# Kernel tuning notes

Hardware: AMD Instinct MI355X
Metric: run time of the kernel (lower is better)

The kernel has to match this reference:

```python
import jax, jax.numpy as jnp
import numpy as np

B, S, E, H = 2, 2048, 1024, 16
D = E // H  # head_dim = 64
EPS = 1e-6


def _angle_decay():
    # angle: 1/10000**linspace(0,1,D//2), each value repeated twice (interleaved)
    a = 1.0 / (10000.0 ** jnp.linspace(0.0, 1.0, D // 2))
    angle = jnp.repeat(a, 2)  # [D]
    decay = jnp.log(1.0 - 2.0 ** (-5.0 - jnp.arange(H, dtype=jnp.float32)))  # [H]
    return angle, decay


def _rel_pos(slen):
    angle, decay = _angle_decay()
    idx = jnp.arange(slen, dtype=jnp.float32)
    sin = jnp.sin(idx[:, None] * angle[None, :])  # [S, D]
    cos = jnp.cos(idx[:, None] * angle[None, :])  # [S, D]
    diff = idx[:, None] - idx[None, :]            # [S, S]
    tril = diff >= 0
    masked = jnp.where(tril, diff, jnp.inf)
    mask = jnp.exp(masked * decay[:, None, None])  # [H, S, S]; exp(-inf)=0 on upper tri
    mask = jnp.nan_to_num(mask)
    mask = mask / jnp.sqrt(jnp.sum(mask, axis=-1, keepdims=True))
    return sin, cos, mask


def _rotate_every_two(x):
    x1 = x[..., ::2]
    x2 = x[..., 1::2]
    return jnp.stack((-x2, x1), axis=-1).reshape(x.shape)


def _theta_shift(x, sin, cos):
    # x: [B, H, S, D]; sin/cos: [S, D] broadcast over B,H
    return x * cos + _rotate_every_two(x) * sin


def setup_inputs() -> dict:
    key = jax.random.key(0)
    ks = jax.random.split(key, 5)
    scale = 1.0 / np.sqrt(E)
    return {
        "x": jax.random.normal(ks[0], (B, S, E), dtype=jnp.float32),
        "Wq": jax.random.normal(ks[1], (E, E), dtype=jnp.float32) * scale,
        "Wk": jax.random.normal(ks[2], (E, E), dtype=jnp.float32) * scale,
        "Wv": jax.random.normal(ks[3], (E, E), dtype=jnp.float32) * scale,
        "Wg": jax.random.normal(ks[4], (E, E), dtype=jnp.float32) * scale,
    }


def reference(x, Wq, Wk, Wv, Wg):
    bsz, tgt_len, _ = x.shape
    sin, cos, mask = _rel_pos(tgt_len)
    scaling = E ** (-0.5)

    q = x @ Wq
    k = (x @ Wk) * scaling
    v = x @ Wv
    g = x @ Wg

    q = q.reshape(bsz, tgt_len, H, D).transpose(0, 2, 1, 3)  # [B,H,S,D]
    k = k.reshape(bsz, tgt_len, H, D).transpose(0, 2, 1, 3)
    vr = v.reshape(bsz, tgt_len, H, D).transpose(0, 2, 1, 3)

    qr = _theta_shift(q, sin, cos)
    kr = _theta_shift(k, sin, cos)

    qk = jnp.einsum("bhqd,bhkd->bhqk", qr, kr) * mask[None]
    denom = jax.lax.stop_gradient(
        jnp.clip(jnp.sum(jnp.abs(qk), axis=-1, keepdims=True), 1.0, 5e4)
    )
    out = jnp.einsum("bhqk,bhkd->bhqd", qk / denom, vr)
    out = out.transpose(0, 2, 1, 3)  # [B,S,H,D]

    # RMSNorm over head_dim (no affine)
    out = out * jax.lax.rsqrt(jnp.mean(out * out, axis=-1, keepdims=True) + EPS)
    out = out.reshape(bsz, tgt_len, E)
    return jax.nn.silu(g) * out
```

## Files before the change

kernel.cpp:

```cpp
#include <hip/hip_runtime.h>

typedef unsigned short u16;
typedef __attribute__((ext_vector_type(8))) __bf16 bf16x8;
typedef __attribute__((ext_vector_type(4))) float f32x4;

#define B_SZ   2
#define S_LEN  2048
#define E_DIM  1024
#define NHEAD  16
#define HD     64
#define KDIM   1024
#define NOUT   4096

__device__ __forceinline__ float bf2f(u16 u){
  union { unsigned int i; float f; } c; c.i = ((unsigned int)u) << 16; return c.f;
}
__device__ __forceinline__ u16 f2bf(float f){
  union { float f; unsigned int i; } c; c.f = f;
  return (u16)((c.i + 0x7FFFu + ((c.i >> 16) & 1u)) >> 16);
}
__device__ __forceinline__ u16 f2bf_fast(float f){
  union { float f; unsigned int i; } c; c.f = f;
  return (u16)((c.i + 0x8000u) >> 16);
}
__device__ __forceinline__ void gl2lds16(const void* g, void* l){
  __builtin_amdgcn_global_load_lds((const __attribute__((address_space(1))) void*)g,
                                   (__attribute__((address_space(3))) void*)l, 16, 0, 0);
}

__global__ __launch_bounds__(256) void castx_kernel(const float* __restrict__ x, u16* __restrict__ xb){
  size_t flat = ((size_t)blockIdx.x * 256 + threadIdx.x) * 16;
  int m7 = (int)((flat >> 10) & 7);
  int cb = (int)((flat >> 3) & 7);
  size_t tile = flat & ~(size_t)63;
  float f[16];
  #pragma unroll
  for (int c = 0; c < 4; c++) *(float4*)&f[c * 4] = *(const float4*)&x[flat + c * 4];
  u16 o[16];
  #pragma unroll
  for (int i = 0; i < 16; i++) o[i] = f2bf(f[i]);
  *(uint4*)&xb[tile + ((cb ^ m7) * 8)]       = *(uint4*)&o[0];
  *(uint4*)&xb[tile + (((cb + 1) ^ m7) * 8)] = *(uint4*)&o[8];
}

__global__ __launch_bounds__(256) void wtrans_kernel(const float* __restrict__ Wq, const float* __restrict__ Wk,
                                                     const float* __restrict__ Wv, const float* __restrict__ Wg,
                                                     u16* __restrict__ WT){
  const float* Ws[4] = {Wq, Wk, Wv, Wg};
  const float* W = Ws[blockIdx.z];
  int n0 = blockIdx.x * 64, k0 = blockIdx.y * 64;
  __shared__ u16 tile[64][66];
  int t = threadIdx.x;
  int r = t >> 2, cg = (t & 3) * 16;
  const float* src = W + (size_t)(k0 + r) * E_DIM + n0 + cg;
  float f[16];
  #pragma unroll
  for (int c = 0; c < 4; c++) *(float4*)&f[c * 4] = *(const float4*)&src[c * 4];
  #pragma unroll
  for (int i = 0; i < 16; i++) tile[r][cg + i] = f2bf(f[i]);
  __syncthreads();
  u16 ov[16];
  #pragma unroll
  for (int i = 0; i < 16; i++) ov[i] = tile[cg + i][r];
  int n7 = r & 7, cb = cg >> 3;
  u16* dst = WT + (size_t)(blockIdx.z * E_DIM + n0 + r) * KDIM + k0;
  *(uint4*)&dst[(cb ^ n7) * 8]       = *(uint4*)&ov[0];
  *(uint4*)&dst[((cb + 1) ^ n7) * 8] = *(uint4*)&ov[8];
}

__global__ __launch_bounds__(256) void gemm_kernel(const u16* __restrict__ A, const u16* __restrict__ Bt,
                                                   u16* __restrict__ C){
  __shared__ __align__(16) u16 As[128 * 64];
  __shared__ __align__(16) u16 Bs[128 * 64];
  int m0 = blockIdx.y * 128, n0 = blockIdx.x * 128;
  int t = threadIdx.x;
  int wave = t >> 6, lane = t & 63;
  int l15 = lane & 15, quad = lane >> 4, h8 = lane & 7;
  int r0 = (wave & 1) * 64, c0 = (wave >> 1) * 64;
  f32x4 acc[4][4];
  #pragma unroll
  for (int i = 0; i < 4; i++)
    #pragma unroll
    for (int j = 0; j < 4; j++) acc[i][j] = (f32x4){0.f, 0.f, 0.f, 0.f};

  for (int k0 = 0; k0 < KDIM; k0 += 64){
    __syncthreads();
    #pragma unroll
    for (int c = 0; c < 4; c++){
      int L = c * 256 + t;
      gl2lds16(A + (size_t)(m0 + (L >> 3)) * KDIM + k0 + (L & 7) * 8, &As[L * 8]);
    }
    #pragma unroll
    for (int c = 0; c < 4; c++){
      int L = c * 256 + t;
      gl2lds16(Bt + (size_t)(n0 + (L >> 3)) * KDIM + k0 + (L & 7) * 8, &Bs[L * 8]);
    }
    __syncthreads();
    #pragma unroll
    for (int kk = 0; kk < 2; kk++){
      bf16x8 a[4], b[4];
      #pragma unroll
      for (int i = 0; i < 4; i++) a[i] = *(const bf16x8*)&As[(r0 + i * 16 + l15) * 64 + ((kk * 4 + quad) ^ h8) * 8];
      #pragma unroll
      for (int j = 0; j < 4; j++) b[j] = *(const bf16x8*)&Bs[(c0 + j * 16 + l15) * 64 + ((kk * 4 + quad) ^ h8) * 8];
      #pragma unroll
      for (int i = 0; i < 4; i++)
        #pragma unroll
        for (int j = 0; j < 4; j++)
          acc[i][j] = __builtin_amdgcn_mfma_f32_16x16x32_bf16(a[i], b[j], acc[i][j], 0, 0, 0);
    }
  }
  #pragma unroll
  for (int i = 0; i < 4; i++){
    int row = m0 + r0 + i * 16 + quad * 4;
    #pragma unroll
    for (int j = 0; j < 4; j++){
      int col = n0 + c0 + j * 16 + l15;
      #pragma unroll
      for (int r = 0; r < 4; r++)
        C[(size_t)(row + r) * NOUT + col] = f2bf(acc[i][j][r]);
    }
  }
}

__global__ __launch_bounds__(256) void shift_kernel(const u16* __restrict__ qkvg,
                                                    u16* __restrict__ qr, u16* __restrict__ kr,
                                                    u16* __restrict__ vt){
  int sb = blockIdx.x, bh = blockIdx.y;
  int s0 = sb * 64;
  int t = threadIdx.x;
  int sl = t >> 2, dg = (t & 3) * 16;
  int s = s0 + sl;
  int h = bh & 15;
  size_t token = (size_t)(bh >> 4) * S_LEN + s;
  size_t base = token * NOUT + h * HD + dg;
  u16 qv[16], kv[16], vv[16];
  *(uint4*)&qv[0] = *(const uint4*)&qkvg[base];
  *(uint4*)&qv[8] = *(const uint4*)&qkvg[base + 8];
  *(uint4*)&kv[0] = *(const uint4*)&qkvg[base + 1024];
  *(uint4*)&kv[8] = *(const uint4*)&qkvg[base + 1024 + 8];
  *(uint4*)&vv[0] = *(const uint4*)&qkvg[base + 2048];
  *(uint4*)&vv[8] = *(const uint4*)&qkvg[base + 2048 + 8];
  u16 qo[16], ko[16];
  #pragma unroll
  for (int i = 0; i < 8; i++){
    int dd = dg + 2 * i;
    float a = exp2f(-(float)(dd >> 1) * (13.287712379549449f / 31.0f));
    float ang = (float)s * a;
    float sn = sinf(ang), cs = cosf(ang);
    float qe = bf2f(qv[2 * i]), qd = bf2f(qv[2 * i + 1]);
    qo[2 * i]     = f2bf(qe * cs - qd * sn);
    qo[2 * i + 1] = f2bf(qd * cs + qe * sn);
    float ke = bf2f(kv[2 * i]) * 0.03125f, kd = bf2f(kv[2 * i + 1]) * 0.03125f;
    ko[2 * i]     = f2bf(ke * cs - kd * sn);
    ko[2 * i + 1] = f2bf(kd * cs + ke * sn);
  }
  size_t dsto = ((size_t)bh * S_LEN + s) * HD;
  *(uint4*)&qr[dsto + dg]     = *(uint4*)&qo[0];
  *(uint4*)&qr[dsto + dg + 8] = *(uint4*)&qo[8];
  int s7 = s & 7, cbk = dg >> 3;
  *(uint4*)&kr[dsto + ((cbk ^ s7) * 8)]       = *(uint4*)&ko[0];
  *(uint4*)&kr[dsto + (((cbk + 1) ^ s7) * 8)] = *(uint4*)&ko[8];
  __shared__ u16 vs[64][66];
  #pragma unroll
  for (int i = 0; i < 16; i++) vs[sl][dg + i] = vv[i];
  __syncthreads();
  int d = t >> 2, jg = (t & 3) * 16;
  u16 ov[16];
  #pragma unroll
  for (int i = 0; i < 16; i++) ov[i] = vs[jg + i][d];
  int d7 = d & 7, cbv = jg >> 3;
  size_t vrow = ((size_t)bh * HD + d) * S_LEN + s0;
  *(uint4*)&vt[vrow + ((cbv ^ d7) * 8)]       = *(uint4*)&ov[0];
  *(uint4*)&vt[vrow + (((cbv + 1) ^ d7) * 8)] = *(uint4*)&ov[8];
}

__global__ __launch_bounds__(256, 2) void retention_kernel(const u16* __restrict__ qr, const u16* __restrict__ kr,
                                                           const u16* __restrict__ vt, const u16* __restrict__ qkvg,
                                                           float* __restrict__ out){
  int bh = blockIdx.x;
  int qb = 15 - (int)blockIdx.y;
  int b = bh >> 4, h = bh & 15;
  int q0 = qb * 128;
  __shared__ __align__(16) u16 Ks[64 * 64];
  __shared__ __align__(16) u16 Vs[64 * 64];
  __shared__ __align__(16) u16 Ps[128 * 72];
  int t = threadIdx.x, wave = t >> 6, lane = t & 63;
  int l15 = lane & 15, quad = lane >> 4, h8 = lane & 7;

  float decay = log1pf(-exp2f(-5.0f - (float)h));
  float negd = -decay;
  float estep = __expf(64.0f * negd);

  int qsE[2]; int rowbase[2];
  #pragma unroll
  for (int e = 0; e < 2; e++){ rowbase[e] = wave * 32 + e * 16; qsE[e] = q0 + rowbase[e]; }

  bf16x8 aqa[2], aqb[2];
  #pragma unroll
  for (int e = 0; e < 2; e++){
    size_t qrow = ((size_t)bh * S_LEN + qsE[e] + l15) * HD;
    aqa[e] = *(const bf16x8*)&qr[qrow + quad * 8];
    aqb[e] = *(const bf16x8*)&qr[qrow + 32 + quad * 8];
  }

  float cf[4];
  #pragma unroll
  for (int ct = 0; ct < 4; ct++) cf[ct] = __expf((float)(ct * 16 + l15) * negd);

  float em1d = expm1f(decay);
  float win_f = 18.0f / negd;
  int win_i = (win_f > 2.1e9f) ? 0x7f000000 : (int)win_f;
  int jmin = q0 - win_i;
  int kb_start = jmin > 0 ? (jmin >> 6) : 0;
  int k0s = kb_start * 64;
  int qi[2][4]; float rf[2][4];
  #pragma unroll
  for (int e = 0; e < 2; e++)
    #pragma unroll
    for (int r = 0; r < 4; r++){
      qi[e][r] = qsE[e] + quad * 4 + r;
      float rowsum = expm1f((float)(qi[e][r] + 1) * decay) / em1d;
      float rinv = rsqrtf(rowsum);
      rf[e][r] = __expf((float)(qi[e][r] - k0s) * decay) * rinv;
    }

  f32x4 o[2][4];
  #pragma unroll
  for (int e = 0; e < 2; e++)
    #pragma unroll
    for (int dt = 0; dt < 4; dt++) o[e][dt] = (f32x4){0.f, 0.f, 0.f, 0.f};
  float babs[2][4] = {{0.f,0.f,0.f,0.f},{0.f,0.f,0.f,0.f}};

  const u16* krbh = kr + (size_t)bh * S_LEN * HD;
  const u16* vtbh = vt + (size_t)bh * HD * S_LEN;
  int kbend = 2 * qb + 1;

  for (int kb = kb_start; kb <= kbend; kb++){
    int k0 = kb * 64;
    __syncthreads();
    #pragma unroll
    for (int c = 0; c < 2; c++){
      int L = c * 256 + t;
      gl2lds16(krbh + (size_t)(k0) * HD + L * 8, &Ks[L * 8]);
    }
    #pragma unroll
    for (int c = 0; c < 2; c++){
      int L = c * 256 + t;
      gl2lds16(vtbh + (size_t)(L >> 3) * S_LEN + k0 + (L & 7) * 8, &Vs[L * 8]);
    }
    __syncthreads();

    bf16x8 bk0[4], bk1[4];
    #pragma unroll
    for (int ct = 0; ct < 4; ct++){
      int rw = (ct * 16 + l15) * 64;
      bk0[ct] = *(const bf16x8*)&Ks[rw + ((quad ^ h8) * 8)];
      bk1[ct] = *(const bf16x8*)&Ks[rw + (((quad + 4) ^ h8) * 8)];
    }
    #pragma unroll
    for (int e = 0; e < 2; e++){
      int qs = qsE[e];
      if (k0 <= qs + 15 && k0 + 63 >= qs - win_i){
        bool diag = (k0 + 64 > qs);
        #pragma unroll
        for (int ct = 0; ct < 4; ct++){
          f32x4 z = (f32x4){0.f, 0.f, 0.f, 0.f};
          z = __builtin_amdgcn_mfma_f32_16x16x32_bf16(aqa[e], bk0[ct], z, 0, 0, 0);
          z = __builtin_amdgcn_mfma_f32_16x16x32_bf16(aqb[e], bk1[ct], z, 0, 0, 0);
          int j = k0 + ct * 16 + l15;
          #pragma unroll
          for (int r = 0; r < 4; r++){
            float p = z[r] * (rf[e][r] * cf[ct]);
            if (diag && j > qi[e][r]) p = 0.f;
            babs[e][r] += fabsf(p);
            Ps[(rowbase[e] + quad * 4 + r) * 72 + ct * 16 + l15] = f2bf_fast(p);
          }
        }
      }
    }
    #pragma unroll
    for (int e = 0; e < 2; e++){
      int qs = qsE[e];
      if (k0 <= qs + 15 && k0 + 63 >= qs - win_i){
        bf16x8 ap0 = *(const bf16x8*)&Ps[(rowbase[e] + l15) * 72 + quad * 8];
        bf16x8 ap1 = *(const bf16x8*)&Ps[(rowbase[e] + l15) * 72 + 32 + quad * 8];
        #pragma unroll
        for (int dt = 0; dt < 4; dt++){
          int rw = (dt * 16 + l15) * 64;
          bf16x8 bv0 = *(const bf16x8*)&Vs[rw + ((quad ^ h8) * 8)];
          bf16x8 bv1 = *(const bf16x8*)&Vs[rw + (((quad + 4) ^ h8) * 8)];
          o[e][dt] = __builtin_amdgcn_mfma_f32_16x16x32_bf16(ap0, bv0, o[e][dt], 0, 0, 0);
          o[e][dt] = __builtin_amdgcn_mfma_f32_16x16x32_bf16(ap1, bv1, o[e][dt], 0, 0, 0);
        }
      }
    }
    #pragma unroll
    for (int e = 0; e < 2; e++)
      #pragma unroll
      for (int r = 0; r < 4; r++) rf[e][r] *= estep;
  }

  #pragma unroll
  for (int e = 0; e < 2; e++){
    float dinv[4];
    #pragma unroll
    for (int r = 0; r < 4; r++){
      float v = babs[e][r];
      v += __shfl_xor(v, 1); v += __shfl_xor(v, 2);
      v += __shfl_xor(v, 4); v += __shfl_xor(v, 8);
      dinv[r] = 1.0f / fminf(fmaxf(v, 1.0f), 50000.0f);
    }
    float ssq[4] = {0.f, 0.f, 0.f, 0.f};
    #pragma unroll
    for (int dt = 0; dt < 4; dt++)
      #pragma unroll
      for (int r = 0; r < 4; r++){
        float v = o[e][dt][r] * dinv[r];
        o[e][dt][r] = v;
        ssq[r] += v * v;
      }
    #pragma unroll
    for (int r = 0; r < 4; r++){
      float v = ssq[r];
      v += __shfl_xor(v, 1); v += __shfl_xor(v, 2);
      v += __shfl_xor(v, 4); v += __shfl_xor(v, 8);
      ssq[r] = rsqrtf(v * (1.0f / 64.0f) + 1e-6f);
    }
    #pragma unroll
    for (int r = 0; r < 4; r++){
      int s = qi[e][r];
      size_t gbase = ((size_t)b * S_LEN + s) * NOUT + 3072 + h * HD;
      size_t obase = ((size_t)b * S_LEN + s) * E_DIM + h * HD;
      #pragma unroll
      for (int dt = 0; dt < 4; dt++){
        int d = dt * 16 + l15;
        float gv = bf2f(qkvg[gbase + d]);
        float sg = gv / (1.0f + __expf(-gv));
        out[obase + d] = o[e][dt][r] * ssq[r] * sg;
      }
    }
  }
}

extern "C" void kernel_launch(void* const* d_in, const int* in_sizes, int n_in,
                              void* d_out, int out_size, void* d_ws, size_t ws_size,
                              hipStream_t stream){
  const float* x  = (const float*)d_in[0];
  const float* Wq = (const float*)d_in[1];
  const float* Wk = (const float*)d_in[2];
  const float* Wv = (const float*)d_in[3];
  const float* Wg = (const float*)d_in[4];
  float* out = (float*)d_out;
  char* ws = (char*)d_ws;
  u16* xb   = (u16*)(ws);
  u16* WT   = (u16*)(ws + (8ull  << 20));
  u16* qkvg = (u16*)(ws + (16ull << 20));
  u16* qrp  = (u16*)(ws);
  u16* vtp  = (u16*)(ws + (8ull  << 20));
  u16* krp  = (u16*)(ws + (48ull << 20));

  castx_kernel    <<<dim3(1024),      256, 0, stream>>>(x, xb);
  wtrans_kernel   <<<dim3(16, 16, 4), 256, 0, stream>>>(Wq, Wk, Wv, Wg, WT);
  gemm_kernel     <<<dim3(32, 32),    256, 0, stream>>>(xb, WT, qkvg);
  shift_kernel    <<<dim3(32, 32),    256, 0, stream>>>(qkvg, qrp, krp, vtp);
  retention_kernel<<<dim3(32, 16),    256, 0, stream>>>(qrp, krp, vtp, qkvg, out);
}
```

Before: 199.4 us.

## Split retention key range across two blocks and combine partials in separate kernel

Splits each retention query block's key loop into two halves (z dimension) so twice as many blocks run, writing partial outputs and abs-sums to workspace. A new combine kernel sums the partials, applies the denominator clamp, RMSNorm and SiLU gate. The gate is copied into a compact buffer during the shift pass, and the QK MFMA operands are swapped so each lane owns one query row, giving packed P stores. This adds workspace traffic and an extra launch in exchange for better load balance and occupancy.

```diff
diff --git a/kernel.cpp b/kernel.cpp
--- a/kernel.cpp
+++ b/kernel.cpp
@@ -1,6 +1,7 @@
 #include <hip/hip_runtime.h>
 
 typedef unsigned short u16;
+typedef unsigned int u32;
 typedef __attribute__((ext_vector_type(8))) __bf16 bf16x8;
 typedef __attribute__((ext_vector_type(4))) float f32x4;
 
@@ -13,14 +14,14 @@
 #define NOUT   4096
 
 __device__ __forceinline__ float bf2f(u16 u){
-  union { unsigned int i; float f; } c; c.i = ((unsigned int)u) << 16; return c.f;
+  union { u32 i; float f; } c; c.i = ((u32)u) << 16; return c.f;
 }
 __device__ __forceinline__ u16 f2bf(float f){
-  union { float f; unsigned int i; } c; c.f = f;
+  union { float f; u32 i; } c; c.f = f;
   return (u16)((c.i + 0x7FFFu + ((c.i >> 16) & 1u)) >> 16);
 }
 __device__ __forceinline__ u16 f2bf_fast(float f){
-  union { float f; unsigned int i; } c; c.f = f;
+  union { float f; u32 i; } c; c.f = f;
   return (u16)((c.i + 0x8000u) >> 16);
 }
 __device__ __forceinline__ void gl2lds16(const void* g, void* l){
@@ -125,7 +126,7 @@
 
 __global__ __launch_bounds__(256) void shift_kernel(const u16* __restrict__ qkvg,
                                                     u16* __restrict__ qr, u16* __restrict__ kr,
-                                                    u16* __restrict__ vt){
+                                                    u16* __restrict__ vt, u16* __restrict__ gc){
   int sb = blockIdx.x, bh = blockIdx.y;
   int s0 = sb * 64;
   int t = threadIdx.x;
@@ -134,13 +135,18 @@
   int h = bh & 15;
   size_t token = (size_t)(bh >> 4) * S_LEN + s;
   size_t base = token * NOUT + h * HD + dg;
-  u16 qv[16], kv[16], vv[16];
+  u16 qv[16], kv[16], vv[16], gv[16];
   *(uint4*)&qv[0] = *(const uint4*)&qkvg[base];
   *(uint4*)&qv[8] = *(const uint4*)&qkvg[base + 8];
   *(uint4*)&kv[0] = *(const uint4*)&qkvg[base + 1024];
   *(uint4*)&kv[8] = *(const uint4*)&qkvg[base + 1024 + 8];
   *(uint4*)&vv[0] = *(const uint4*)&qkvg[base + 2048];
   *(uint4*)&vv[8] = *(const uint4*)&qkvg[base + 2048 + 8];
+  *(uint4*)&gv[0] = *(const uint4*)&qkvg[base + 3072];
+  *(uint4*)&gv[8] = *(const uint4*)&qkvg[base + 3072 + 8];
+  size_t gdst = token * E_DIM + h * HD + dg;
+  *(uint4*)&gc[gdst]     = *(uint4*)&gv[0];
+  *(uint4*)&gc[gdst + 8] = *(uint4*)&gv[8];
   u16 qo[16], ko[16];
   #pragma unroll
   for (int i = 0; i < 8; i++){
@@ -176,11 +182,12 @@
 }
 
 __global__ __launch_bounds__(256, 2) void retention_kernel(const u16* __restrict__ qr, const u16* __restrict__ kr,
-                                                           const u16* __restrict__ vt, const u16* __restrict__ qkvg,
-                                                           float* __restrict__ out){
+                                                           const u16* __restrict__ vt,
+                                                           float* __restrict__ pO, float* __restrict__ pBa){
   int bh = blockIdx.x;
   int qb = 15 - (int)blockIdx.y;
-  int b = bh >> 4, h = bh & 15;
+  int z  = blockIdx.z;
+  int h = bh & 15;
   int q0 = qb * 128;
   __shared__ __align__(16) u16 Ks[64 * 64];
   __shared__ __align__(16) u16 Vs[64 * 64];
@@ -192,57 +199,61 @@
   float negd = -decay;
   float estep = __expf(64.0f * negd);
 
-  int qsE[2]; int rowbase[2];
-  #pragma unroll
-  for (int e = 0; e < 2; e++){ rowbase[e] = wave * 32 + e * 16; qsE[e] = q0 + rowbase[e]; }
-
-  bf16x8 aqa[2], aqb[2];
+  int qsE[2], rowb[2];
+  #pragma unroll
+  for (int e = 0; e < 2; e++){ rowb[e] = wave * 32 + e * 16; qsE[e] = q0 + rowb[e]; }
+
+  bf16x8 qB[2][2];
   #pragma unroll
   for (int e = 0; e < 2; e++){
     size_t qrow = ((size_t)bh * S_LEN + qsE[e] + l15) * HD;
-    aqa[e] = *(const bf16x8*)&qr[qrow + quad * 8];
-    aqb[e] = *(const bf16x8*)&qr[qrow + 32 + quad * 8];
-  }
-
-  float cf[4];
-  #pragma unroll
-  for (int ct = 0; ct < 4; ct++) cf[ct] = __expf((float)(ct * 16 + l15) * negd);
-
-  float em1d = expm1f(decay);
+    qB[e][0] = *(const bf16x8*)&qr[qrow + quad * 8];
+    qB[e][1] = *(const bf16x8*)&qr[qrow + 32 + quad * 8];
+  }
+
   float win_f = 18.0f / negd;
   int win_i = (win_f > 2.1e9f) ? 0x7f000000 : (int)win_f;
-  int jmin = q0 - win_i;
-  int kb_start = jmin > 0 ? (jmin >> 6) : 0;
-  int k0s = kb_start * 64;
-  int qi[2][4]; float rf[2][4];
+  int z_lo = z ? (qb + 1) : 0;
+  int z_hi = z ? (2 * qb + 1) : qb;
+  int kb_lo = z_lo;
+  {
+    int jmin = q0 - win_i;
+    if (jmin > z_lo * 64){ int wlo = jmin >> 6; kb_lo = wlo > z_lo ? wlo : z_lo; }
+  }
+  int k0s = kb_lo * 64;
+
+  float em1d = expm1f(decay);
+  float rfE[2]; int iE[2];
+  #pragma unroll
+  for (int e = 0; e < 2; e++){
+    int i = qsE[e] + l15;
+    iE[e] = i;
+    float rowsum = expm1f((float)(i + 1) * decay) / em1d;
+    rfE[e] = __expf((float)(i - k0s) * decay) * rsqrtf(rowsum);
+  }
+  float e1 = __expf(negd);
+  float c16 = __expf(negd * 16.0f);
+  float cbr[4];
+  cbr[0] = __expf(negd * (float)(quad * 4));
+  cbr[1] = cbr[0] * e1; cbr[2] = cbr[1] * e1; cbr[3] = cbr[2] * e1;
+
+  f32x4 o[2][4];
   #pragma unroll
   for (int e = 0; e < 2; e++)
     #pragma unroll
-    for (int r = 0; r < 4; r++){
-      qi[e][r] = qsE[e] + quad * 4 + r;
-      float rowsum = expm1f((float)(qi[e][r] + 1) * decay) / em1d;
-      float rinv = rsqrtf(rowsum);
-      rf[e][r] = __expf((float)(qi[e][r] - k0s) * decay) * rinv;
-    }
-
-  f32x4 o[2][4];
-  #pragma unroll
-  for (int e = 0; e < 2; e++)
-    #pragma unroll
     for (int dt = 0; dt < 4; dt++) o[e][dt] = (f32x4){0.f, 0.f, 0.f, 0.f};
-  float babs[2][4] = {{0.f,0.f,0.f,0.f},{0.f,0.f,0.f,0.f}};
+  float babs[2] = {0.f, 0.f};
 
   const u16* krbh = kr + (size_t)bh * S_LEN * HD;
   const u16* vtbh = vt + (size_t)bh * HD * S_LEN;
-  int kbend = 2 * qb + 1;
-
-  for (int kb = kb_start; kb <= kbend; kb++){
+
+  for (int kb = kb_lo; kb <= z_hi; kb++){
     int k0 = kb * 64;
     __syncthreads();
     #pragma unroll
     for (int c = 0; c < 2; c++){
       int L = c * 256 + t;
-      gl2lds16(krbh + (size_t)(k0) * HD + L * 8, &Ks[L * 8]);
+      gl2lds16(krbh + (size_t)k0 * HD + L * 8, &Ks[L * 8]);
     }
     #pragma unroll
     for (int c = 0; c < 2; c++){
@@ -251,31 +262,36 @@
     }
     __syncthreads();
 
-    bf16x8 bk0[4], bk1[4];
+    bf16x8 kA0[4], kA1[4];
     #pragma unroll
     for (int ct = 0; ct < 4; ct++){
       int rw = (ct * 16 + l15) * 64;
-      bk0[ct] = *(const bf16x8*)&Ks[rw + ((quad ^ h8) * 8)];
-      bk1[ct] = *(const bf16x8*)&Ks[rw + (((quad + 4) ^ h8) * 8)];
+      kA0[ct] = *(const bf16x8*)&Ks[rw + ((quad ^ h8) * 8)];
+      kA1[ct] = *(const bf16x8*)&Ks[rw + (((quad + 4) ^ h8) * 8)];
     }
     #pragma unroll
     for (int e = 0; e < 2; e++){
       int qs = qsE[e];
       if (k0 <= qs + 15 && k0 + 63 >= qs - win_i){
         bool diag = (k0 + 64 > qs);
+        float cf[4] = {cbr[0], cbr[1], cbr[2], cbr[3]};
         #pragma unroll
         for (int ct = 0; ct < 4; ct++){
-          f32x4 z = (f32x4){0.f, 0.f, 0.f, 0.f};
-          z = __builtin_amdgcn_mfma_f32_16x16x32_bf16(aqa[e], bk0[ct], z, 0, 0, 0);
-          z = __builtin_amdgcn_mfma_f32_16x16x32_bf16(aqb[e], bk1[ct], z, 0, 0, 0);
-          int j = k0 + ct * 16 + l15;
+          f32x4 zacc = (f32x4){0.f, 0.f, 0.f, 0.f};
+          zacc = __builtin_amdgcn_mfma_f32_16x16x32_bf16(kA0[ct], qB[e][0], zacc, 0, 0, 0);
+          zacc = __builtin_amdgcn_mfma_f32_16x16x32_bf16(kA1[ct], qB[e][1], zacc, 0, 0, 0);
+          u16 pk[4];
           #pragma unroll
           for (int r = 0; r < 4; r++){
-            float p = z[r] * (rf[e][r] * cf[ct]);
-            if (diag && j > qi[e][r]) p = 0.f;
-            babs[e][r] += fabsf(p);
-            Ps[(rowbase[e] + quad * 4 + r) * 72 + ct * 16 + l15] = f2bf_fast(p);
+            float p = zacc[r] * (rfE[e] * cf[r]);
+            if (diag && (k0 + ct * 16 + quad * 4 + r) > iE[e]) p = 0.f;
+            babs[e] += fabsf(p);
+            pk[r] = f2bf_fast(p);
+            cf[r] *= c16;
           }
+          u32 lo = (u32)pk[0] | ((u32)pk[1] << 16);
+          u32 hi = (u32)pk[2] | ((u32)pk[3] << 16);
+          *(uint2*)&Ps[(rowb[e] + l15) * 72 + ct * 16 + quad * 4] = make_uint2(lo, hi);
         }
       }
     }
@@ -283,64 +299,76 @@
     for (int e = 0; e < 2; e++){
       int qs = qsE[e];
       if (k0 <= qs + 15 && k0 + 63 >= qs - win_i){
-        bf16x8 ap0 = *(const bf16x8*)&Ps[(rowbase[e] + l15) * 72 + quad * 8];
-        bf16x8 ap1 = *(const bf16x8*)&Ps[(rowbase[e] + l15) * 72 + 32 + quad * 8];
+        bf16x8 pB0 = *(const bf16x8*)&Ps[(rowb[e] + l15) * 72 + quad * 8];
+        bf16x8 pB1 = *(const bf16x8*)&Ps[(rowb[e] + l15) * 72 + 32 + quad * 8];
         #pragma unroll
         for (int dt = 0; dt < 4; dt++){
           int rw = (dt * 16 + l15) * 64;
-          bf16x8 bv0 = *(const bf16x8*)&Vs[rw + ((quad ^ h8) * 8)];
-          bf16x8 bv1 = *(const bf16x8*)&Vs[rw + (((quad + 4) ^ h8) * 8)];
-          o[e][dt] = __builtin_amdgcn_mfma_f32_16x16x32_bf16(ap0, bv0, o[e][dt], 0, 0, 0);
-          o[e][dt] = __builtin_amdgcn_mfma_f32_16x16x32_bf16(ap1, bv1, o[e][dt], 0, 0, 0);
+          bf16x8 vA0 = *(const bf16x8*)&Vs[rw + ((quad ^ h8) * 8)];
+          bf16x8 vA1 = *(const bf16x8*)&Vs[rw + (((quad + 4) ^ h8) * 8)];
+          o[e][dt] = __builtin_amdgcn_mfma_f32_16x16x32_bf16(vA0, pB0, o[e][dt], 0, 0, 0);
+          o[e][dt] = __builtin_amdgcn_mfma_f32_16x16x32_bf16(vA1, pB1, o[e][dt], 0, 0, 0);
         }
       }
     }
     #pragma unroll
-    for (int e = 0; e < 2; e++)
-      #pragma unroll
-      for (int r = 0; r < 4; r++) rf[e][r] *= estep;
-  }
-
+    for (int e = 0; e < 2; e++) rfE[e] *= estep;
+  }
+
+  size_t slot = ((size_t)bh * 16 + qb) * 2 + z;
+  float* po = pO + slot * (4 * 128 * 16);
   #pragma unroll
   for (int e = 0; e < 2; e++){
-    float dinv[4];
-    #pragma unroll
-    for (int r = 0; r < 4; r++){
-      float v = babs[e][r];
-      v += __shfl_xor(v, 1); v += __shfl_xor(v, 2);
-      v += __shfl_xor(v, 4); v += __shfl_xor(v, 8);
-      dinv[r] = 1.0f / fminf(fmaxf(v, 1.0f), 50000.0f);
-    }
-    float ssq[4] = {0.f, 0.f, 0.f, 0.f};
+    float bsum = babs[e];
+    bsum += __shfl_xor(bsum, 16);
+    bsum += __shfl_xor(bsum, 32);
+    if (quad == 0) pBa[slot * 128 + rowb[e] + l15] = bsum;
     #pragma unroll
     for (int dt = 0; dt < 4; dt++)
-      #pragma unroll
-      for (int r = 0; r < 4; r++){
-        float v = o[e][dt][r] * dinv[r];
-        o[e][dt][r] = v;
-        ssq[r] += v * v;
-      }
-    #pragma unroll
-    for (int r = 0; r < 4; r++){
-      float v = ssq[r];
-      v += __shfl_xor(v, 1); v += __shfl_xor(v, 2);
-      v += __shfl_xor(v, 4); v += __shfl_xor(v, 8);
-      ssq[r] = rsqrtf(v * (1.0f / 64.0f) + 1e-6f);
-    }
-    #pragma unroll
-    for (int r = 0; r < 4; r++){
-      int s = qi[e][r];
-      size_t gbase = ((size_t)b * S_LEN + s) * NOUT + 3072 + h * HD;
-      size_t obase = ((size_t)b * S_LEN + s) * E_DIM + h * HD;
-      #pragma unroll
-      for (int dt = 0; dt < 4; dt++){
-        int d = dt * 16 + l15;
-        float gv = bf2f(qkvg[gbase + d]);
-        float sg = gv / (1.0f + __expf(-gv));
-        out[obase + d] = o[e][dt][r] * ssq[r] * sg;
-      }
-    }
-  }
+      *(float4*)&po[(dt * 128 + rowb[e] + l15) * 16 + quad * 4] = *(float4*)&o[e][dt];
+  }
+}
+
+__global__ __launch_bounds__(128) void combine_kernel(const float* __restrict__ pO, const float* __restrict__ pBa,
+                                                      const u16* __restrict__ gc, float* __restrict__ out){
+  int bh = blockIdx.x, qb = blockIdx.y;
+  int b = bh >> 4, h = bh & 15;
+  int i = threadIdx.x;
+  int s = qb * 128 + i;
+  size_t s2 = ((size_t)bh * 16 + qb) * 2;
+  const float* p0 = pO + s2 * 8192;
+  const float* p1 = p0 + 8192;
+  float v[64];
+  #pragma unroll
+  for (int dt = 0; dt < 4; dt++)
+    #pragma unroll
+    for (int c = 0; c < 4; c++){
+      float4 a  = *(const float4*)&p0[(dt * 128 + i) * 16 + c * 4];
+      float4 bb = *(const float4*)&p1[(dt * 128 + i) * 16 + c * 4];
+      int d = dt * 16 + c * 4;
+      v[d + 0] = a.x + bb.x; v[d + 1] = a.y + bb.y;
+      v[d + 2] = a.z + bb.z; v[d + 3] = a.w + bb.w;
+    }
+  float bsum = pBa[s2 * 128 + i] + pBa[(s2 + 1) * 128 + i];
+  float dinv = 1.0f / fminf(fmaxf(bsum, 1.0f), 50000.0f);
+  float ssq = 0.f;
+  #pragma unroll
+  for (int d = 0; d < 64; d++){ v[d] *= dinv; ssq += v[d] * v[d]; }
+  float rms = rsqrtf(ssq * (1.0f / 64.0f) + 1e-6f);
+  size_t gbase = ((size_t)b * S_LEN + s) * E_DIM + h * HD;
+  u16 gu[64];
+  #pragma unroll
+  for (int c = 0; c < 8; c++) *(uint4*)&gu[c * 8] = *(const uint4*)&gc[gbase + c * 8];
+  float ov[64];
+  #pragma unroll
+  for (int d = 0; d < 64; d++){
+    float gv = bf2f(gu[d]);
+    float sg = gv / (1.0f + __expf(-gv));
+    ov[d] = v[d] * rms * sg;
+  }
+  float* obase = out + ((size_t)b * S_LEN + s) * E_DIM + h * HD;
+  #pragma unroll
+  for (int c = 0; c < 16; c++) *(float4*)&obase[c * 4] = *(float4*)&ov[c * 4];
 }
 
 extern "C" void kernel_launch(void* const* d_in, const int* in_sizes, int n_in,
@@ -353,16 +381,20 @@
   const float* Wg = (const float*)d_in[4];
   float* out = (float*)d_out;
   char* ws = (char*)d_ws;
-  u16* xb   = (u16*)(ws);
-  u16* WT   = (u16*)(ws + (8ull  << 20));
-  u16* qkvg = (u16*)(ws + (16ull << 20));
-  u16* qrp  = (u16*)(ws);
-  u16* vtp  = (u16*)(ws + (8ull  << 20));
-  u16* krp  = (u16*)(ws + (48ull << 20));
-
-  castx_kernel    <<<dim3(1024),      256, 0, stream>>>(x, xb);
-  wtrans_kernel   <<<dim3(16, 16, 4), 256, 0, stream>>>(Wq, Wk, Wv, Wg, WT);
-  gemm_kernel     <<<dim3(32, 32),    256, 0, stream>>>(xb, WT, qkvg);
-  shift_kernel    <<<dim3(32, 32),    256, 0, stream>>>(qkvg, qrp, krp, vtp);
-  retention_kernel<<<dim3(32, 16),    256, 0, stream>>>(qrp, krp, vtp, qkvg, out);
-}
+  u16*   xb   = (u16*)(ws);
+  u16*   WT   = (u16*)(ws + (8ull  << 20));
+  u16*   qkvg = (u16*)(ws + (16ull << 20));
+  u16*   qrp  = (u16*)(ws);
+  u16*   vtp  = (u16*)(ws + (8ull  << 20));
+  float* pO   = (float*)(ws + (16ull << 20));
+  u16*   krp  = (u16*)(ws + (48ull << 20));
+  u16*   gcp  = (u16*)(ws + (56ull << 20));
+  float* pBa  = (float*)(ws + (64ull << 20));
+
+  castx_kernel    <<<dim3(1024),       256, 0, stream>>>(x, xb);
+  wtrans_kernel   <<<dim3(16, 16, 4),  256, 0, stream>>>(Wq, Wk, Wv, Wg, WT);
+  gemm_kernel     <<<dim3(32, 32),     256, 0, stream>>>(xb, WT, qkvg);
+  shift_kernel    <<<dim3(32, 32),     256, 0, stream>>>(qkvg, qrp, krp, vtp, gcp);
+  retention_kernel<<<dim3(32, 16, 2),  256, 0, stream>>>(qrp, krp, vtp, pO, pBa);
+  combine_kernel  <<<dim3(32, 16),     128, 0, stream>>>(pO, pBa, gcp, out);
+}
```

Measured after the change: 195.1 us. -2.1%, faster.
